# Performance work log

Measured on AMD Instinct MI355X. Metric: run time of the kernel, lower is better.

The kernel has to match this reference:

```python
import jax, jax.numpy as jnp
import numpy as np

MASK_THRESHOLD = 0.53
NUM_CC_ITERS = 10


def _convert(prob, coords, size0, size1, thr):
    # prob: [N,1,h,w] float; coords: [2,N,1,h,w] int (coords[0]=x, coords[1]=y)
    N = prob.shape[0]
    labels = jnp.broadcast_to(
        jnp.arange(1, N + 1, dtype=jnp.float32)[:, None, None, None], prob.shape
    ).ravel()
    p = prob.ravel()
    x = coords[0].ravel()
    y = coords[1].ravel()
    key = x * size1 + y
    OOB = size0 * size1  # sentinel for sub-threshold pixels
    keym = jnp.where(p >= thr, key, OOB)
    # torch: stable argsort prob desc, then stable argsort key asc ==
    # lexicographic (key asc, prob desc, original index asc)
    order = jnp.lexsort((jnp.arange(p.size), -p, keym))
    ks = keym[order]
    ls = labels[order]
    first = jnp.concatenate([jnp.array([True]), ks[1:] != ks[:-1]])
    win = first & (ks < OOB)
    scatter_idx = jnp.where(win, ks, OOB)
    flat = jnp.zeros(size0 * size1, jnp.float32).at[scatter_idx].set(ls, mode='drop')
    return flat.reshape(size0, size1)


def _find_connected_components(adj):
    K = adj.shape[0]
    eye = jnp.eye(K, dtype=adj.dtype)
    M = adj + eye
    out = jnp.linalg.matrix_power(M, NUM_CC_ITERS)
    col = jnp.arange(K, dtype=adj.dtype)[:, None]  # col[i,j] = i
    out_col_idx = ((out > 1).astype(adj.dtype) - eye) * col
    maxes = jnp.argmax(out_col_idx, axis=0) * (jnp.max(out_col_idx, axis=0) > 0)
    maxes = jnp.maximum(maxes + 1, jnp.arange(K) + 1)
    tentative = jnp.stack([jnp.arange(K) + 1, maxes]).astype(jnp.float32)
    return jnp.concatenate([jnp.zeros((2, 1), jnp.float32), tentative], axis=1)  # [2, K+1]


def setup_inputs() -> dict:
    key = jax.random.key(0)
    k1, k2, k3 = jax.random.split(key, 3)
    N, h, w = 512, 96, 96
    size0 = size1 = 1024
    prob_input = jax.random.uniform(k1, (N, 1, h, w), dtype=jnp.float32)
    coords_input = jax.random.randint(k2, (2, N, 1, h, w), 0, size0, dtype=jnp.int64)
    # sparse symmetric binary adjacency between the N instances
    a = (jax.random.uniform(k3, (N, N)) < 0.002).astype(jnp.float32)
    adjacency = jnp.maximum(a, a.T) * (1.0 - jnp.eye(N, dtype=jnp.float32))
    return {
        'prob_input': prob_input,
        'coords_input': coords_input,
        'adjacency': adjacency,
        'size0': size0,
        'size1': size1,
    }


def reference(prob_input, coords_input, adjacency, size0, size1):
    label_map = _convert(prob_input, coords_input, size0, size1, MASK_THRESHOLD)
    remapping = _find_connected_components(adjacency)  # [2, N+1]
    # apply the connected-component remapping to the label map (gather)
    out = remapping[1][label_map.astype(jnp.int32)]
    return out
```

## Files before the change

kernel.cpp:

```cpp
#include <hip/hip_runtime.h>
#include <math.h>

#define MASK_THR 0.53f
#define NBLKA 512
#define BLKA_THR 1024
#define BFIN_THR 1024
#define CAPB 32
#define NBK 256
#define BSH 12
#define BMSK 4095
#define OVFC 64
#define DEGCAP 64

typedef unsigned long long u64;

__global__ __launch_bounds__(BLKA_THR) void k_binA(
        const float* __restrict__ prob, const int* __restrict__ coords,
        const float* __restrict__ adj,
        unsigned* __restrict__ cnt, u64* __restrict__ buf,
        unsigned* __restrict__ ovfcnt, u64* __restrict__ ovf,
        unsigned* __restrict__ deg, int* __restrict__ cols,
        int NE, int HW4, int NB1, const int* __restrict__ d_size1,
        int i4PerBlk, int nbuck, int N) {
    __shared__ u64 slab[NBK * CAPB];
    __shared__ unsigned hist[NBK];
    __shared__ unsigned lcnt, ocnt;
    int tid = threadIdx.x, blk = blockIdx.x;
    for (int i = tid; i < NBK; i += BLKA_THR) hist[i] = 0u;
    if (tid == 0) { lcnt = 0u; ocnt = 0u; }
    __syncthreads();
    if (blk < N) {
        for (int c = tid; c < N; c += BLKA_THR)
            if (adj[(size_t)blk * N + c] != 0.0f) {
                unsigned pos = atomicAdd(&lcnt, 1u);
                if (pos < DEGCAP) cols[(size_t)blk * DEGCAP + pos] = c;
            }
    }
    int size1 = *d_size1;
    int NE4 = NE >> 2;
    int i4Base = blk * i4PerBlk;
    int i4End = min(i4Base + i4PerBlk, NE4);
    for (int i4 = i4Base + tid; i4 < i4End; i4 += BLKA_THR) {
        float4 p = ((const float4*)prob)[i4];
        float pv[4] = {p.x, p.y, p.z, p.w};
        bool any = (pv[0] >= MASK_THR) | (pv[1] >= MASK_THR) |
                   (pv[2] >= MASK_THR) | (pv[3] >= MASK_THR);
        if (!any) continue;
        int4 x = ((const int4*)coords)[i4];
        int4 y = ((const int4*)(coords + NE))[i4];
        unsigned n = (unsigned)i4 / (unsigned)HW4;
        unsigned tie = (unsigned)(NB1 - (int)n);
        int   xv[4] = {x.x, x.y, x.z, x.w};
        int   yv[4] = {y.x, y.y, y.z, y.w};
#pragma unroll
        for (int e = 0; e < 4; ++e)
            if (pv[e] >= MASK_THR) {
                unsigned key = (unsigned)(xv[e] * size1 + yv[e]);
                unsigned b = key >> BSH;
                unsigned v = ((__float_as_uint(pv[e]) & 0x7FFFFFu) << 9) | tie;
                unsigned pos = atomicAdd(&hist[b], 1u);
                if (pos < CAPB)
                    slab[b * CAPB + pos] = ((u64)(key & BMSK) << 32) | v;
                else {
                    unsigned g = atomicAdd(&ocnt, 1u);
                    if (g < OVFC) ovf[(size_t)blk * OVFC + g] =
                        ((u64)key << 32) | v;
                }
            }
    }
    __syncthreads();
    if (tid == 0) {
        ovfcnt[blk] = min(ocnt, (unsigned)OVFC);
        if (blk < N) deg[blk] = min(lcnt, (unsigned)DEGCAP);
    }
    for (int b = tid; b < nbuck; b += BLKA_THR) {
        unsigned c = hist[b];
        if (c > CAPB) c = CAPB;
        cnt[(size_t)blk * NBK + b] = c;
        hist[b] = c;
    }
    __syncthreads();
    for (int j = tid; j < NBK * CAPB; j += BLKA_THR) {
        int b = j >> 5, s = j & (CAPB - 1);
        if (s < (int)hist[b])
            buf[((size_t)blk * NBK + b) * CAPB + s] = slab[j];
    }
}

__global__ __launch_bounds__(256) void k_walk(
        const unsigned* __restrict__ deg, const int* __restrict__ cols,
        float* __restrict__ rmap, int N) {
    __shared__ float v0[512], v1[512];
    __shared__ int red[4];
    int i = blockIdx.x, tid = threadIdx.x;
    for (int j = tid; j < N; j += 256) v0[j] = (j == i) ? 1.0f : 0.0f;
    __syncthreads();
    float* cur = v0; float* nxt = v1;
    for (int it = 0; it < 10; ++it) {
        for (int j = tid; j < N; j += 256) {
            float s = cur[j];
            unsigned d = deg[j];
            const int* cj = cols + (size_t)j * DEGCAP;
            for (unsigned k = 0; k < d; ++k) s += cur[cj[k]];
            nxt[j] = s;
        }
        __syncthreads();
        float* t = cur; cur = nxt; nxt = t;
    }
    int best = i;
    for (int j = tid; j < N; j += 256)
        if (j != i && cur[j] > 1.0f && j > best) best = j;
    for (int off = 32; off; off >>= 1) {
        int o = __shfl_down(best, off);
        if (o > best) best = o;
    }
    if ((tid & 63) == 0) red[tid >> 6] = best;
    __syncthreads();
    if (tid == 0) {
        for (int w = 1; w < 4; ++w) if (red[w] > best) best = red[w];
        rmap[i] = (float)(best + 1);
    }
}

__global__ __launch_bounds__(BFIN_THR) void k_binBfin(
        const unsigned* __restrict__ cnt, const u64* __restrict__ buf,
        const unsigned* __restrict__ ovfcnt, const u64* __restrict__ ovf,
        const float* __restrict__ rmap, float* __restrict__ out,
        int total, int NB1) {
    __shared__ unsigned bins[1 << BSH];
    __shared__ unsigned lc[NBLKA];
    __shared__ unsigned oc[NBLKA];
    int b = blockIdx.x, tid = threadIdx.x;
    for (int i = tid; i < (1 << BSH); i += BFIN_THR) bins[i] = 0u;
    for (int s = tid; s < NBLKA; s += BFIN_THR) {
        lc[s] = cnt[(size_t)s * NBK + b];
        oc[s] = ovfcnt[s];
    }
    __syncthreads();
    for (int j = tid; j < NBLKA * CAPB; j += BFIN_THR) {
        int s = j >> 5, slot = j & (CAPB - 1);
        if (slot < (int)lc[s]) {
            u64 kv = buf[((size_t)s * NBK + b) * CAPB + slot];
            atomicMax(&bins[(unsigned)(kv >> 32)], (unsigned)kv);
        }
    }
    for (int j = tid; j < NBLKA * OVFC; j += BFIN_THR) {
        int s = j / OVFC, e = j % OVFC;
        if (e < (int)oc[s]) {
            u64 kv = ovf[(size_t)s * OVFC + e];
            unsigned key = (unsigned)(kv >> 32);
            if ((int)(key >> BSH) == b)
                atomicMax(&bins[key & BMSK], (unsigned)kv);
        }
    }
    __syncthreads();
    int base = b << BSH;
    for (int i = tid; i < (1 << BSH); i += BFIN_THR) {
        int g = base + i;
        if (g < total) {
            unsigned v = bins[i];
            out[g] = v ? rmap[NB1 - (int)(v & 0x1FFu)] : 0.0f;
        }
    }
}

__global__ __launch_bounds__(256) void k_scatter(
        const float* __restrict__ prob, const int* __restrict__ coords,
        unsigned* __restrict__ packed, int NE, int HW4, int NB1,
        const int* __restrict__ d_size1) {
    int i4 = blockIdx.x * blockDim.x + threadIdx.x;
    if (i4 * 4 >= NE) return;
    int size1 = *d_size1;
    float4 p = ((const float4*)prob)[i4];
    int4 x = ((const int4*)coords)[i4];
    int4 y = ((const int4*)(coords + NE))[i4];
    unsigned n = (unsigned)i4 / (unsigned)HW4;
    unsigned tie = (unsigned)(NB1 - (int)n);
    float pv[4] = {p.x, p.y, p.z, p.w};
    int   xv[4] = {x.x, x.y, x.z, x.w};
    int   yv[4] = {y.x, y.y, y.z, y.w};
#pragma unroll
    for (int e = 0; e < 4; ++e)
        if (pv[e] >= MASK_THR) {
            unsigned v = ((__float_as_uint(pv[e]) & 0x7FFFFFu) << 9) | tie;
            atomicMax(&packed[xv[e] * size1 + yv[e]], v);
        }
}

__global__ void k_edges(const float* __restrict__ adj, unsigned* __restrict__ deg,
                        int* __restrict__ cols, int N) {
    __shared__ unsigned lcnt;
    int r = blockIdx.x, tid = threadIdx.x;
    if (tid == 0) lcnt = 0u;
    __syncthreads();
    for (int c = tid; c < N; c += blockDim.x)
        if (adj[(size_t)r * N + c] != 0.0f) {
            unsigned pos = atomicAdd(&lcnt, 1u);
            if (pos < DEGCAP) cols[(size_t)r * DEGCAP + pos] = c;
        }
    __syncthreads();
    if (tid == 0) deg[r] = min(lcnt, (unsigned)DEGCAP);
}

__global__ void k_finalize(const unsigned* __restrict__ packed,
                           const float* __restrict__ rmap,
                           float* __restrict__ out, int total, int NB1) {
    int i4 = blockIdx.x * blockDim.x + threadIdx.x;
    if (i4 * 4 >= total) return;
    uint4 u = ((const uint4*)packed)[i4];
    unsigned v[4] = {u.x, u.y, u.z, u.w};
    float o[4];
#pragma unroll
    for (int e = 0; e < 4; ++e)
        o[e] = v[e] ? rmap[NB1 - (int)(v[e] & 0x1FFu)] : 0.0f;
    ((float4*)out)[i4] = make_float4(o[0], o[1], o[2], o[3]);
}

extern "C" void kernel_launch(void* const* d_in, const int* in_sizes, int n_in,
                              void* d_out, int out_size, void* d_ws, size_t ws_size,
                              hipStream_t stream) {
    const float* prob   = (const float*)d_in[0];
    const int*   coords = (const int*)d_in[1];
    const float* adj    = (const float*)d_in[2];
    const int*   dsz1   = (const int*)d_in[4];

    const int NE = in_sizes[0];
    const int NN = in_sizes[2];
    int N = (int)(sqrt((double)NN) + 0.5);
    const int HW = NE / N;
    const int total = out_size;
    const int NB1 = N - 1;
    const int nbuck = (total + BMSK) >> BSH;

    char* ws = (char*)d_ws;
    const size_t slabB = (size_t)NBLKA * NBK * CAPB * 8;
    const size_t cntB  = (size_t)NBLKA * NBK * 4;
    const size_t ocB   = (size_t)NBLKA * 4;
    const size_t ovfB  = (size_t)NBLKA * OVFC * 8;
    const size_t colB  = (size_t)512 * DEGCAP * 4;
    const size_t degB  = 512 * 4;
    const size_t rmapB = 512 * 4;
    const size_t needBin = slabB + cntB + ocB + ovfB + colB + degB + rmapB + 256;

    bool binOK = (nbuck <= NBK) && (N <= 512) && (N <= NBLKA) &&
                 (NE % 4 == 0) && (HW % 4 == 0) && (ws_size >= needBin);

    if (binOK) {
        size_t off = 0;
        u64* buf = (u64*)(ws + off); off += slabB;
        unsigned* cnt = (unsigned*)(ws + off); off += cntB;
        unsigned* ovfcnt = (unsigned*)(ws + off); off += ocB;
        u64* ovf = (u64*)(ws + off); off += ovfB;
        int* cols = (int*)(ws + off); off += colB;
        unsigned* deg = (unsigned*)(ws + off); off += degB;
        float* rmap = (float*)(ws + off);

        int NE4 = NE / 4;
        int i4PerBlk = (NE4 + NBLKA - 1) / NBLKA;
        k_binA<<<NBLKA, BLKA_THR, 0, stream>>>(
            prob, coords, adj, cnt, buf, ovfcnt, ovf, deg, cols,
            NE, HW / 4, NB1, dsz1, i4PerBlk, nbuck, N);

        k_walk<<<N, 256, 0, stream>>>(deg, cols, rmap, N);

        k_binBfin<<<nbuck, BFIN_THR, 0, stream>>>(cnt, buf, ovfcnt, ovf, rmap,
                                                  (float*)d_out, total, NB1);
    } else {
        unsigned* packed = (unsigned*)ws;
        size_t off = (size_t)total * 4;
        int* cols = (int*)(ws + off); off += colB;
        unsigned* deg = (unsigned*)(ws + off); off += degB;
        float* rmap = (float*)(ws + off);

        hipMemsetAsync(packed, 0, (size_t)total * 4, stream);
        k_scatter<<<(NE / 4 + 255) / 256, 256, 0, stream>>>(
            prob, coords, packed, NE, HW / 4, NB1, dsz1);
        k_edges<<<N, 256, 0, stream>>>(adj, deg, cols, N);
        k_walk<<<N, 256, 0, stream>>>(deg, cols, rmap, N);
        k_finalize<<<(total / 4 + 255) / 256, 256, 0, stream>>>(
            packed, rmap, (float*)d_out, total, NB1);
    }
}
```

Measured before the change: 54.44 us.

## Transpose bin buffer to bucket-major and drop per-slot counts with zero-filled slabs

The first kernel now zero-fills its shared slab and writes all slots into a bucket-major buffer, so the per-block count array is no longer needed. The finalize kernel then streams each bucket's contiguous region with 16-byte loads and applies atomicMax on every entry, relying on zero entries being harmless. This removes the count array traffic and the scattered, conditional loads in the finalize stage. In exchange both kernels always move the full slab (including empty slots), and slab zeroing adds shared-memory stores.

```diff
diff --git a/kernel.cpp b/kernel.cpp
--- a/kernel.cpp
+++ b/kernel.cpp
@@ -17,16 +17,17 @@
 __global__ __launch_bounds__(BLKA_THR) void k_binA(
         const float* __restrict__ prob, const int* __restrict__ coords,
         const float* __restrict__ adj,
-        unsigned* __restrict__ cnt, u64* __restrict__ buf,
+        u64* __restrict__ buf,
         unsigned* __restrict__ ovfcnt, u64* __restrict__ ovf,
         unsigned* __restrict__ deg, int* __restrict__ cols,
         int NE, int HW4, int NB1, const int* __restrict__ d_size1,
-        int i4PerBlk, int nbuck, int N) {
+        int i4PerBlk, int N) {
     __shared__ u64 slab[NBK * CAPB];
     __shared__ unsigned hist[NBK];
     __shared__ unsigned lcnt, ocnt;
     int tid = threadIdx.x, blk = blockIdx.x;
     for (int i = tid; i < NBK; i += BLKA_THR) hist[i] = 0u;
+    for (int i = tid; i < NBK * CAPB; i += BLKA_THR) slab[i] = 0ull;
     if (tid == 0) { lcnt = 0u; ocnt = 0u; }
     __syncthreads();
     if (blk < N) {
@@ -73,17 +74,9 @@
         ovfcnt[blk] = min(ocnt, (unsigned)OVFC);
         if (blk < N) deg[blk] = min(lcnt, (unsigned)DEGCAP);
     }
-    for (int b = tid; b < nbuck; b += BLKA_THR) {
-        unsigned c = hist[b];
-        if (c > CAPB) c = CAPB;
-        cnt[(size_t)blk * NBK + b] = c;
-        hist[b] = c;
-    }
-    __syncthreads();
     for (int j = tid; j < NBK * CAPB; j += BLKA_THR) {
         int b = j >> 5, s = j & (CAPB - 1);
-        if (s < (int)hist[b])
-            buf[((size_t)blk * NBK + b) * CAPB + s] = slab[j];
+        buf[((size_t)b * NBLKA + blk) * CAPB + s] = slab[j];
     }
 }
 
@@ -123,26 +116,22 @@
 }
 
 __global__ __launch_bounds__(BFIN_THR) void k_binBfin(
-        const unsigned* __restrict__ cnt, const u64* __restrict__ buf,
+        const u64* __restrict__ buf,
         const unsigned* __restrict__ ovfcnt, const u64* __restrict__ ovf,
         const float* __restrict__ rmap, float* __restrict__ out,
         int total, int NB1) {
     __shared__ unsigned bins[1 << BSH];
-    __shared__ unsigned lc[NBLKA];
     __shared__ unsigned oc[NBLKA];
     int b = blockIdx.x, tid = threadIdx.x;
     for (int i = tid; i < (1 << BSH); i += BFIN_THR) bins[i] = 0u;
-    for (int s = tid; s < NBLKA; s += BFIN_THR) {
-        lc[s] = cnt[(size_t)s * NBK + b];
-        oc[s] = ovfcnt[s];
-    }
-    __syncthreads();
-    for (int j = tid; j < NBLKA * CAPB; j += BFIN_THR) {
-        int s = j >> 5, slot = j & (CAPB - 1);
-        if (slot < (int)lc[s]) {
-            u64 kv = buf[((size_t)s * NBK + b) * CAPB + slot];
-            atomicMax(&bins[(unsigned)(kv >> 32)], (unsigned)kv);
-        }
+    for (int s = tid; s < NBLKA; s += BFIN_THR) oc[s] = ovfcnt[s];
+    __syncthreads();
+    const uint4* src = (const uint4*)(buf + (size_t)b * NBLKA * CAPB);
+    const int n4 = NBLKA * CAPB / 2;
+    for (int j = tid; j < n4; j += BFIN_THR) {
+        uint4 u = src[j];
+        atomicMax(&bins[u.y], u.x);
+        atomicMax(&bins[u.w], u.z);
     }
     for (int j = tid; j < NBLKA * OVFC; j += BFIN_THR) {
         int s = j / OVFC, e = j % OVFC;
@@ -234,13 +223,12 @@
 
     char* ws = (char*)d_ws;
     const size_t slabB = (size_t)NBLKA * NBK * CAPB * 8;
-    const size_t cntB  = (size_t)NBLKA * NBK * 4;
     const size_t ocB   = (size_t)NBLKA * 4;
     const size_t ovfB  = (size_t)NBLKA * OVFC * 8;
     const size_t colB  = (size_t)512 * DEGCAP * 4;
     const size_t degB  = 512 * 4;
     const size_t rmapB = 512 * 4;
-    const size_t needBin = slabB + cntB + ocB + ovfB + colB + degB + rmapB + 256;
+    const size_t needBin = slabB + ocB + ovfB + colB + degB + rmapB + 256;
 
     bool binOK = (nbuck <= NBK) && (N <= 512) && (N <= NBLKA) &&
                  (NE % 4 == 0) && (HW % 4 == 0) && (ws_size >= needBin);
@@ -248,7 +236,6 @@
     if (binOK) {
         size_t off = 0;
         u64* buf = (u64*)(ws + off); off += slabB;
-        unsigned* cnt = (unsigned*)(ws + off); off += cntB;
         unsigned* ovfcnt = (unsigned*)(ws + off); off += ocB;
         u64* ovf = (u64*)(ws + off); off += ovfB;
         int* cols = (int*)(ws + off); off += colB;
@@ -258,12 +245,12 @@
         int NE4 = NE / 4;
         int i4PerBlk = (NE4 + NBLKA - 1) / NBLKA;
         k_binA<<<NBLKA, BLKA_THR, 0, stream>>>(
-            prob, coords, adj, cnt, buf, ovfcnt, ovf, deg, cols,
-            NE, HW / 4, NB1, dsz1, i4PerBlk, nbuck, N);
+            prob, coords, adj, buf, ovfcnt, ovf, deg, cols,
+            NE, HW / 4, NB1, dsz1, i4PerBlk, N);
 
         k_walk<<<N, 256, 0, stream>>>(deg, cols, rmap, N);
 
-        k_binBfin<<<nbuck, BFIN_THR, 0, stream>>>(cnt, buf, ovfcnt, ovf, rmap,
+        k_binBfin<<<nbuck, BFIN_THR, 0, stream>>>(buf, ovfcnt, ovf, rmap,
                                                   (float*)d_out, total, NB1);
     } else {
         unsigned* packed = (unsigned*)ws;
```

New measurement: 56.52 us. 3.8% more time.

## Transpose bin buffer to bucket-major layout with nontemporal and vectorized accesses

Applied to the files above, without the earlier changes.

Reorders the intermediate bin buffer and counts from source-block-major to bucket-major, so each finalize block reads one contiguous region. The per-slot counts shrink to 16-bit and the finalize pass reads two key/value pairs per 16-byte vector load. Nontemporal loads and stores are added for the streaming inputs, the buffer writes and the output. The transposed layout makes the producer's writes more scattered across buckets, and count writes now have a stride of NBLKA, which may hurt coalescing in the first kernel.

```diff
diff --git a/kernel.cpp b/kernel.cpp
--- a/kernel.cpp
+++ b/kernel.cpp
@@ -13,15 +13,18 @@
 #define DEGCAP 64
 
 typedef unsigned long long u64;
+typedef float    fx4 __attribute__((ext_vector_type(4)));
+typedef int      ix4 __attribute__((ext_vector_type(4)));
+typedef unsigned ux4 __attribute__((ext_vector_type(4)));
 
 __global__ __launch_bounds__(BLKA_THR) void k_binA(
         const float* __restrict__ prob, const int* __restrict__ coords,
         const float* __restrict__ adj,
-        unsigned* __restrict__ cnt, u64* __restrict__ buf,
+        u64* __restrict__ buf, unsigned short* __restrict__ cnt,
         unsigned* __restrict__ ovfcnt, u64* __restrict__ ovf,
         unsigned* __restrict__ deg, int* __restrict__ cols,
         int NE, int HW4, int NB1, const int* __restrict__ d_size1,
-        int i4PerBlk, int nbuck, int N) {
+        int i4PerBlk, int N) {
     __shared__ u64 slab[NBK * CAPB];
     __shared__ unsigned hist[NBK];
     __shared__ unsigned lcnt, ocnt;
@@ -41,13 +44,13 @@
     int i4Base = blk * i4PerBlk;
     int i4End = min(i4Base + i4PerBlk, NE4);
     for (int i4 = i4Base + tid; i4 < i4End; i4 += BLKA_THR) {
-        float4 p = ((const float4*)prob)[i4];
+        fx4 p = __builtin_nontemporal_load(&((const fx4*)prob)[i4]);
         float pv[4] = {p.x, p.y, p.z, p.w};
         bool any = (pv[0] >= MASK_THR) | (pv[1] >= MASK_THR) |
                    (pv[2] >= MASK_THR) | (pv[3] >= MASK_THR);
         if (!any) continue;
-        int4 x = ((const int4*)coords)[i4];
-        int4 y = ((const int4*)(coords + NE))[i4];
+        ix4 x = __builtin_nontemporal_load(&((const ix4*)coords)[i4]);
+        ix4 y = __builtin_nontemporal_load(&((const ix4*)(coords + NE))[i4]);
         unsigned n = (unsigned)i4 / (unsigned)HW4;
         unsigned tie = (unsigned)(NB1 - (int)n);
         int   xv[4] = {x.x, x.y, x.z, x.w};
@@ -73,17 +76,18 @@
         ovfcnt[blk] = min(ocnt, (unsigned)OVFC);
         if (blk < N) deg[blk] = min(lcnt, (unsigned)DEGCAP);
     }
-    for (int b = tid; b < nbuck; b += BLKA_THR) {
+    for (int b = tid; b < NBK; b += BLKA_THR) {
         unsigned c = hist[b];
         if (c > CAPB) c = CAPB;
-        cnt[(size_t)blk * NBK + b] = c;
+        cnt[(size_t)b * NBLKA + blk] = (unsigned short)c;
         hist[b] = c;
     }
     __syncthreads();
     for (int j = tid; j < NBK * CAPB; j += BLKA_THR) {
         int b = j >> 5, s = j & (CAPB - 1);
         if (s < (int)hist[b])
-            buf[((size_t)blk * NBK + b) * CAPB + s] = slab[j];
+            __builtin_nontemporal_store(
+                slab[j], &buf[((size_t)b * NBLKA + blk) * CAPB + s]);
     }
 }
 
@@ -123,25 +127,29 @@
 }
 
 __global__ __launch_bounds__(BFIN_THR) void k_binBfin(
-        const unsigned* __restrict__ cnt, const u64* __restrict__ buf,
+        const u64* __restrict__ buf, const unsigned short* __restrict__ cnt,
         const unsigned* __restrict__ ovfcnt, const u64* __restrict__ ovf,
         const float* __restrict__ rmap, float* __restrict__ out,
         int total, int NB1) {
     __shared__ unsigned bins[1 << BSH];
-    __shared__ unsigned lc[NBLKA];
+    __shared__ unsigned short lc[NBLKA];
     __shared__ unsigned oc[NBLKA];
     int b = blockIdx.x, tid = threadIdx.x;
     for (int i = tid; i < (1 << BSH); i += BFIN_THR) bins[i] = 0u;
     for (int s = tid; s < NBLKA; s += BFIN_THR) {
-        lc[s] = cnt[(size_t)s * NBK + b];
+        lc[s] = cnt[(size_t)b * NBLKA + s];
         oc[s] = ovfcnt[s];
     }
     __syncthreads();
-    for (int j = tid; j < NBLKA * CAPB; j += BFIN_THR) {
-        int s = j >> 5, slot = j & (CAPB - 1);
-        if (slot < (int)lc[s]) {
-            u64 kv = buf[((size_t)s * NBK + b) * CAPB + slot];
-            atomicMax(&bins[(unsigned)(kv >> 32)], (unsigned)kv);
+    const int W = CAPB / 2;
+    const ux4* base = (const ux4*)(buf + (size_t)b * NBLKA * CAPB);
+    for (int j = tid; j < NBLKA * W; j += BFIN_THR) {
+        int s = j / W, w = j % W;
+        int c = (int)lc[s];
+        if (2 * w < c) {
+            ux4 u = __builtin_nontemporal_load(&base[s * W + w]);
+            atomicMax(&bins[u.y], u.x);
+            if (2 * w + 1 < c) atomicMax(&bins[u.w], u.z);
         }
     }
     for (int j = tid; j < NBLKA * OVFC; j += BFIN_THR) {
@@ -154,12 +162,13 @@
         }
     }
     __syncthreads();
-    int base = b << BSH;
+    int bse = b << BSH;
     for (int i = tid; i < (1 << BSH); i += BFIN_THR) {
-        int g = base + i;
+        int g = bse + i;
         if (g < total) {
             unsigned v = bins[i];
-            out[g] = v ? rmap[NB1 - (int)(v & 0x1FFu)] : 0.0f;
+            float o = v ? rmap[NB1 - (int)(v & 0x1FFu)] : 0.0f;
+            __builtin_nontemporal_store(o, &out[g]);
         }
     }
 }
@@ -234,7 +243,7 @@
 
     char* ws = (char*)d_ws;
     const size_t slabB = (size_t)NBLKA * NBK * CAPB * 8;
-    const size_t cntB  = (size_t)NBLKA * NBK * 4;
+    const size_t cntB  = (size_t)NBK * NBLKA * 2;
     const size_t ocB   = (size_t)NBLKA * 4;
     const size_t ovfB  = (size_t)NBLKA * OVFC * 8;
     const size_t colB  = (size_t)512 * DEGCAP * 4;
@@ -248,7 +257,7 @@
     if (binOK) {
         size_t off = 0;
         u64* buf = (u64*)(ws + off); off += slabB;
-        unsigned* cnt = (unsigned*)(ws + off); off += cntB;
+        unsigned short* cnt = (unsigned short*)(ws + off); off += cntB;
         unsigned* ovfcnt = (unsigned*)(ws + off); off += ocB;
         u64* ovf = (u64*)(ws + off); off += ovfB;
         int* cols = (int*)(ws + off); off += colB;
@@ -258,12 +267,12 @@
         int NE4 = NE / 4;
         int i4PerBlk = (NE4 + NBLKA - 1) / NBLKA;
         k_binA<<<NBLKA, BLKA_THR, 0, stream>>>(
-            prob, coords, adj, cnt, buf, ovfcnt, ovf, deg, cols,
-            NE, HW / 4, NB1, dsz1, i4PerBlk, nbuck, N);
+            prob, coords, adj, buf, cnt, ovfcnt, ovf, deg, cols,
+            NE, HW / 4, NB1, dsz1, i4PerBlk, N);
 
         k_walk<<<N, 256, 0, stream>>>(deg, cols, rmap, N);
 
-        k_binBfin<<<nbuck, BFIN_THR, 0, stream>>>(cnt, buf, ovfcnt, ovf, rmap,
+        k_binBfin<<<nbuck, BFIN_THR, 0, stream>>>(buf, cnt, ovfcnt, ovf, rmap,
                                                   (float*)d_out, total, NB1);
     } else {
         unsigned* packed = (unsigned*)ws;
@@ -272,7 +281,7 @@
         unsigned* deg = (unsigned*)(ws + off); off += degB;
         float* rmap = (float*)(ws + off);
 
-        hipMemsetAsync(packed, 0, (size_t)total * 4, stream);
+        (void)hipMemsetAsync(packed, 0, (size_t)total * 4, stream);
         k_scatter<<<(NE / 4 + 255) / 256, 256, 0, stream>>>(
             prob, coords, packed, NE, HW / 4, NB1, dsz1);
         k_edges<<<N, 256, 0, stream>>>(adj, deg, cols, N);
```

After: 56.21 us, median of 2. 3.2% more time.
